# Kernel optimization log

Measured on AMD Instinct MI355X. Metric: run time of the kernel, lower is better.

Reference implementation:

```python
import jax, jax.numpy as jnp
import numpy as np

N = 524288      # total nodes across batched subgraphs
E = 4194304     # total edges (avg degree ~8)
B = 4096        # number of subgraphs (links)
H = 32          # hidden_dim
L = 3           # num_layers
K = 30          # sort-pool k
MAXZ = 1000     # max DRNL label
EPS = 1e-5      # BatchNorm eps


def setup_inputs() -> dict:
    key = jax.random.key(0)
    ks = jax.random.split(key, 12)
    x_z = jax.random.randint(ks[0], (N,), 0, MAXZ + 1, dtype=jnp.int32)
    edge_index = jax.random.randint(ks[1], (2, E), 0, N, dtype=jnp.int32)
    batch = jnp.sort(jax.random.randint(ks[2], (N,), 0, B, dtype=jnp.int32))
    # parameters
    emb = jax.random.normal(ks[3], (MAXZ + 1, H), jnp.float32) * 0.1
    Wc = jax.random.normal(ks[4], (L, H, H), jnp.float32) * (1.0 / np.sqrt(H))
    bc = jnp.zeros((L, H), jnp.float32)
    gamma = jnp.ones((L, H), jnp.float32)
    beta = jnp.zeros((L, H), jnp.float32)
    rmean = jax.random.normal(ks[5], (L, H), jnp.float32) * 0.1
    rvar = 1.0 + 0.1 * jax.random.uniform(ks[6], (L, H), jnp.float32)
    W1 = jax.random.normal(ks[7], (K * H, H), jnp.float32) * (1.0 / np.sqrt(K * H))
    b1 = jnp.zeros((H,), jnp.float32)
    W2 = jax.random.normal(ks[8], (H, H // 2), jnp.float32) * (1.0 / np.sqrt(H))
    b2 = jnp.zeros((H // 2,), jnp.float32)
    W3 = jax.random.normal(ks[9], (H // 2, 1), jnp.float32) * (1.0 / np.sqrt(H // 2))
    b3 = jnp.zeros((1,), jnp.float32)
    return dict(x_z=x_z, edge_index=edge_index, batch=batch, emb=emb, Wc=Wc, bc=bc,
                gamma=gamma, beta=beta, rmean=rmean, rvar=rvar,
                W1=W1, b1=b1, W2=W2, b2=b2, W3=W3, b3=b3)


def reference(x_z, edge_index, batch, emb, Wc, bc, gamma, beta, rmean, rvar,
              W1, b1, W2, b2, W3, b3):
    src, dst = edge_index[0], edge_index[1]
    # GCN symmetric normalization with added self-loops: deg[i] = in_deg(i) + 1
    deg = jnp.zeros((N,), jnp.float32).at[dst].add(1.0) + 1.0
    dinv = jax.lax.rsqrt(deg)
    enorm = dinv[src] * dinv[dst]          # [E]
    self_norm = dinv * dinv                # [N] self-loop coefficient

    x = emb[x_z]                           # [N, H]
    for i in range(L):
        h = x @ Wc[i]                      # [N, H]
        agg = (jnp.zeros_like(h).at[dst].add(h[src] * enorm[:, None])
               + h * self_norm[:, None] + bc[i])
        # BatchNorm1d (eval: running stats) + ReLU; dropout is identity in eval
        xn = (agg - rmean[i]) * jax.lax.rsqrt(rvar[i] + EPS) * gamma[i] + beta[i]
        x = jax.nn.relu(xn)

    # SortAggregation: per-graph sort desc by last channel, keep top-K, zero-pad
    order = jnp.lexsort((-x[:, -1], batch))   # group by graph, desc by last feat
    xs = x[order]
    bs = batch[order]
    counts = jnp.zeros((B,), jnp.int32).at[batch].add(1)
    starts = jnp.concatenate([jnp.zeros((1,), jnp.int32), jnp.cumsum(counts)[:-1]])
    rank = jnp.arange(N, dtype=jnp.int32) - starts[bs]
    slot = jnp.where(rank < K, rank, K)       # overflow -> dummy slot K
    pooled = jnp.zeros((B, K + 1, H), x.dtype).at[bs, slot].set(xs)
    pooled = pooled[:, :K].reshape(B, K * H)  # [B, K*H]

    h1 = jax.nn.relu(pooled @ W1 + b1)
    h2 = jax.nn.relu(h1 @ W2 + b2)
    out = (h2 @ W3 + b3)[:, 0]                # [B]
    return out
```

## Files before the change

kernel.cpp:

```cpp
#include <hip/hip_runtime.h>
#include <hip/hip_bf16.h>
#include <stdint.h>

#define N_NODES 524288
#define N_EDGES 4194304
#define N_GRAPHS 4096
#define HDIM 32
#define NLAYERS 3
#define KPOOL 30
#define MAXC 1024

#define NBUCKET 1024
#define BSHIFT 9
#define NPB 512
#define NCOPY 8
#define HIST_SZ (NBUCKET * NCOPY)
#define CAP 6144

typedef unsigned long long ull;

__global__ void k_hist(const int* __restrict__ dst, int* __restrict__ ghist,
                       int* __restrict__ deg) {
    __shared__ int lh[NBUCKET];
    int t = threadIdx.x;
    for (int i = t; i < NBUCKET; i += 256) lh[i] = 0;
    __syncthreads();
    int base = blockIdx.x * 2048;
    for (int i = t; i < 2048; i += 256) {
        int d = dst[base + i];
        atomicAdd(&lh[d >> BSHIFT], 1);
        atomicAdd(&deg[d], 1);
    }
    __syncthreads();
    int c = blockIdx.x & 7;
    for (int i = t; i < NBUCKET; i += 256) {
        int v = lh[i];
        if (v) atomicAdd(&ghist[i * NCOPY + c], v);
    }
}

__global__ void k_dinv(const int* __restrict__ deg, float* __restrict__ dinv) {
    int n = blockIdx.x * 256 + threadIdx.x;
    if (n < N_NODES) {
        float d = (float)(deg[n] + 1);
        float sq = (float)sqrt((double)d);
        dinv[n] = (float)(1.0 / (double)sq);
    }
}

__global__ void k_scan8k(const int* __restrict__ ghist, int* __restrict__ gbase,
                         int* __restrict__ cur) {
    __shared__ int tmp[256];
    int t = threadIdx.x;
    int loc[32];
    int s = 0;
    for (int k = 0; k < 32; ++k) { loc[k] = ghist[t * 32 + k]; s += loc[k]; }
    tmp[t] = s;
    __syncthreads();
    for (int d = 1; d < 256; d <<= 1) {
        int a = (t >= d) ? tmp[t - d] : 0;
        __syncthreads();
        tmp[t] += a;
        __syncthreads();
    }
    int run = tmp[t] - s;
    for (int k = 0; k < 32; ++k) {
        gbase[t * 32 + k] = run;
        cur[t * 32 + k] = run;
        run += loc[k];
    }
}

__global__ void k_bin(const int* __restrict__ src, const int* __restrict__ dst,
                      int* __restrict__ cur, ull* __restrict__ stage) {
    int base = blockIdx.x * 2048;
    int c = blockIdx.x & 7;
    int t = threadIdx.x;
    for (int i = t; i < 2048; i += 256) {
        int e = base + i;
        int d = dst[e];
        int b = d >> BSHIFT;
        int pos = atomicAdd(&cur[b * NCOPY + c], 1);
        ull rec = ((ull)(unsigned)src[e] << 32)
                | (unsigned)(((d & (NPB - 1)) << 22) | e);
        stage[pos] = rec;
    }
}

__global__ void k_build(const ull* __restrict__ stage, const int* __restrict__ gbase,
                        const float* __restrict__ dinv,
                        int* __restrict__ offs, ull* __restrict__ csr2,
                        int* __restrict__ perm) {
    __shared__ ull grp[CAP];
    __shared__ int cnt[NPB];
    __shared__ int sstart[NPB];
    __shared__ int cur[NPB];
    __shared__ int tmp[256];
    int b = blockIdx.x, t = threadIdx.x;
    int s0 = gbase[b * NCOPY];
    int s1 = (b == NBUCKET - 1) ? N_EDGES : gbase[(b + 1) * NCOPY];
    int win = s1 - s0;
    for (int j = t; j < NPB; j += 256) cnt[j] = 0;
    __syncthreads();
    const unsigned* lo32 = (const unsigned*)stage;
    for (int i = t; i < win; i += 256) {
        unsigned k = lo32[2 * (s0 + i)];
        atomicAdd(&cnt[(k >> 22) & (NPB - 1)], 1);
    }
    __syncthreads();
    int j0 = 2 * t, j1 = 2 * t + 1;
    int a0 = cnt[j0], a1 = cnt[j1];
    int s = a0 + a1;
    tmp[t] = s;
    __syncthreads();
    for (int d = 1; d < 256; d <<= 1) {
        int a = (t >= d) ? tmp[t - d] : 0;
        __syncthreads();
        tmp[t] += a;
        __syncthreads();
    }
    int run = tmp[t] - s;
    sstart[j0] = run;      sstart[j1] = run + a0;
    cur[j0] = run;         cur[j1] = run + a0;
    offs[b * NPB + j0] = s0 + run;
    offs[b * NPB + j1] = s0 + run + a0;
    if (b == NBUCKET - 1 && t == 255) offs[N_NODES] = N_EDGES;
    __syncthreads();

    if (win <= CAP) {
        for (int i = t; i < win; i += 256) {
            ull v = stage[s0 + i];
            unsigned k = (unsigned)v;
            int pos = atomicAdd(&cur[(k >> 22) & (NPB - 1)], 1);
            grp[pos] = v;
        }
        __syncthreads();
        for (int jj = 0; jj < 2; ++jj) {
            int j = 2 * t + jj;
            int beg = sstart[j], end = beg + cnt[j];
            for (int i = beg + 1; i < end; ++i) {
                ull v = grp[i];
                unsigned kv = (unsigned)v;
                int q = i - 1;
                while (q >= beg && (unsigned)grp[q] > kv) { grp[q + 1] = grp[q]; --q; }
                grp[q + 1] = v;
            }
        }
        __syncthreads();
        int i = t;
        for (; i + 768 < win; i += 1024) {
            ull v0 = grp[i], v1 = grp[i + 256], v2 = grp[i + 512], v3 = grp[i + 768];
            float d0 = dinv[(int)(v0 >> 32)];
            float d1 = dinv[(int)(v1 >> 32)];
            float d2 = dinv[(int)(v2 >> 32)];
            float d3 = dinv[(int)(v3 >> 32)];
            csr2[s0 + i]       = (v0 & 0xffffffff00000000ull) | (unsigned)__float_as_uint(d0);
            csr2[s0 + i + 256] = (v1 & 0xffffffff00000000ull) | (unsigned)__float_as_uint(d1);
            csr2[s0 + i + 512] = (v2 & 0xffffffff00000000ull) | (unsigned)__float_as_uint(d2);
            csr2[s0 + i + 768] = (v3 & 0xffffffff00000000ull) | (unsigned)__float_as_uint(d3);
        }
        for (; i < win; i += 256) {
            ull v = grp[i];
            float dv = dinv[(int)(v >> 32)];
            csr2[s0 + i] = (v & 0xffffffff00000000ull) | (unsigned)__float_as_uint(dv);
        }
    } else {
        for (int i = t; i < win; i += 256) {
            ull v = stage[s0 + i];
            unsigned k = (unsigned)v;
            int pos = s0 + atomicAdd(&cur[(k >> 22) & (NPB - 1)], 1);
            csr2[pos] = v;
        }
        __syncthreads();
        for (int jj = 0; jj < 2; ++jj) {
            int j = 2 * t + jj;
            int beg = s0 + sstart[j], end = beg + cnt[j];
            for (int i = beg + 1; i < end; ++i) {
                ull v = csr2[i];
                unsigned kv = (unsigned)v;
                int q = i - 1;
                while (q >= beg && (unsigned)csr2[q] > kv) { csr2[q + 1] = csr2[q]; --q; }
                csr2[q + 1] = v;
            }
        }
        __syncthreads();
        for (int i = t; i < win; i += 256) {
            ull v = csr2[s0 + i];
            float dv = dinv[(int)(v >> 32)];
            csr2[s0 + i] = (v & 0xffffffff00000000ull) | (unsigned)__float_as_uint(dv);
        }
    }
    __syncthreads();
    for (int jj = 0; jj < 2; ++jj) {
        int j = 2 * t + jj;
        int dj = cnt[j];
        int r = 0;
        for (int k = 0; k < NPB; ++k) {
            int dk = cnt[k];
            r += (dk < dj) || (dk == dj && k < j);
        }
        perm[b * NPB + r] = b * NPB + j;
    }
}

__global__ void k_bnprep(const float* __restrict__ rvar, float* __restrict__ rs) {
    int i = threadIdx.x;
    if (i < NLAYERS * HDIM) {
        float rv = __fadd_rn(rvar[i], 1e-5f);
        float sq = (float)sqrt((double)rv);
        rs[i] = (float)(1.0 / (double)sq);
    }
}

__global__ void k_embed_mm(const int* __restrict__ xz, const float* __restrict__ emb,
                           const float* __restrict__ Wc, float* __restrict__ h) {
    __shared__ float Wl[HDIM * HDIM];
    __shared__ float xt[256];
    int t = threadIdx.x;
    int base = blockIdx.x * 256;
    for (int i = t; i < HDIM * HDIM; i += 256) Wl[i] = Wc[i];
    {
        int gid = base + t;
        int n = gid >> 5, c = gid & 31;
        xt[t] = emb[xz[n] * HDIM + c];
    }
    __syncthreads();
    int nl = t >> 5, c = t & 31;
    float acc = 0.0f;
#pragma unroll
    for (int k = 0; k < HDIM; ++k) acc = __fmaf_rn(xt[nl * HDIM + k], Wl[k * HDIM + c], acc);
    h[base + t] = acc;
}

__device__ __forceinline__ float agg_phase(const float* __restrict__ h,
                                           const float* __restrict__ dinv,
                                           const int* __restrict__ offs,
                                           const ull* __restrict__ csr2,
                                           const float* __restrict__ bc,
                                           const float* __restrict__ rmean,
                                           const float* __restrict__ rs,
                                           const float* __restrict__ gamma,
                                           const float* __restrict__ beta,
                                           int n, int c) {
    float di = dinv[n];
    float hself = h[n * HDIM + c];
    float accE = 0.0f;
    int beg = offs[n], end = offs[n + 1];
    int i = beg;
    for (; i + 8 <= end; i += 8) {
        ull r0 = csr2[i];
        ull r1 = csr2[i + 1];
        ull r2 = csr2[i + 2];
        ull r3 = csr2[i + 3];
        ull r4 = csr2[i + 4];
        ull r5 = csr2[i + 5];
        ull r6 = csr2[i + 6];
        ull r7 = csr2[i + 7];
        float h0 = h[(int)(r0 >> 32) * HDIM + c];
        float h1 = h[(int)(r1 >> 32) * HDIM + c];
        float h2 = h[(int)(r2 >> 32) * HDIM + c];
        float h3 = h[(int)(r3 >> 32) * HDIM + c];
        float h4 = h[(int)(r4 >> 32) * HDIM + c];
        float h5 = h[(int)(r5 >> 32) * HDIM + c];
        float h6 = h[(int)(r6 >> 32) * HDIM + c];
        float h7 = h[(int)(r7 >> 32) * HDIM + c];
        accE = __fadd_rn(accE, __fmul_rn(h0, __fmul_rn(__uint_as_float((unsigned)r0), di)));
        accE = __fadd_rn(accE, __fmul_rn(h1, __fmul_rn(__uint_as_float((unsigned)r1), di)));
        accE = __fadd_rn(accE, __fmul_rn(h2, __fmul_rn(__uint_as_float((unsigned)r2), di)));
        accE = __fadd_rn(accE, __fmul_rn(h3, __fmul_rn(__uint_as_float((unsigned)r3), di)));
        accE = __fadd_rn(accE, __fmul_rn(h4, __fmul_rn(__uint_as_float((unsigned)r4), di)));
        accE = __fadd_rn(accE, __fmul_rn(h5, __fmul_rn(__uint_as_float((unsigned)r5), di)));
        accE = __fadd_rn(accE, __fmul_rn(h6, __fmul_rn(__uint_as_float((unsigned)r6), di)));
        accE = __fadd_rn(accE, __fmul_rn(h7, __fmul_rn(__uint_as_float((unsigned)r7), di)));
    }
    for (; i + 4 <= end; i += 4) {
        ull r0 = csr2[i];
        ull r1 = csr2[i + 1];
        ull r2 = csr2[i + 2];
        ull r3 = csr2[i + 3];
        float h0 = h[(int)(r0 >> 32) * HDIM + c];
        float h1 = h[(int)(r1 >> 32) * HDIM + c];
        float h2 = h[(int)(r2 >> 32) * HDIM + c];
        float h3 = h[(int)(r3 >> 32) * HDIM + c];
        accE = __fadd_rn(accE, __fmul_rn(h0, __fmul_rn(__uint_as_float((unsigned)r0), di)));
        accE = __fadd_rn(accE, __fmul_rn(h1, __fmul_rn(__uint_as_float((unsigned)r1), di)));
        accE = __fadd_rn(accE, __fmul_rn(h2, __fmul_rn(__uint_as_float((unsigned)r2), di)));
        accE = __fadd_rn(accE, __fmul_rn(h3, __fmul_rn(__uint_as_float((unsigned)r3), di)));
    }
    for (; i < end; ++i) {
        ull r = csr2[i];
        float hv = h[(int)(r >> 32) * HDIM + c];
        float dv = __uint_as_float((unsigned)r);
        accE = __fadd_rn(accE, __fmul_rn(hv, __fmul_rn(dv, di)));
    }
    float sn = __fmul_rn(di, di);
    float t1 = __fmul_rn(hself, sn);
    float a2 = __fadd_rn(accE, t1);
    float a3 = __fadd_rn(a2, bc[c]);
    float tt = __fsub_rn(a3, rmean[c]);
    float u  = __fmul_rn(tt, rs[c]);
    float v  = __fmul_rn(u, gamma[c]);
    float xn = __fadd_rn(v, beta[c]);
    return (xn > 0.0f) ? xn : 0.0f;
}

__global__ void k_agg_mm(const float* __restrict__ h, const float* __restrict__ dinv,
                         const int* __restrict__ offs, const ull* __restrict__ csr2,
                         const int* __restrict__ perm,
                         const float* __restrict__ bc, const float* __restrict__ rmean,
                         const float* __restrict__ rs, const float* __restrict__ gamma,
                         const float* __restrict__ beta,
                         const float* __restrict__ Wnext, float* __restrict__ hout) {
    __shared__ float Wl[HDIM * HDIM];
    __shared__ float xt[256];
    __shared__ int nodes[8];
    int t = threadIdx.x;
    for (int i = t; i < HDIM * HDIM; i += 256) Wl[i] = Wnext[i];
    if (t < 8) nodes[t] = perm[blockIdx.x * 8 + t];
    __syncthreads();
    int slot = t >> 5, c = t & 31;
    int n = nodes[slot];
    xt[t] = agg_phase(h, dinv, offs, csr2, bc, rmean, rs, gamma, beta, n, c);
    __syncthreads();
    float acc = 0.0f;
#pragma unroll
    for (int k = 0; k < HDIM; ++k) acc = __fmaf_rn(xt[slot * HDIM + k], Wl[k * HDIM + c], acc);
    hout[n * HDIM + c] = acc;
}

__global__ void k_agg_last(const float* __restrict__ h, const float* __restrict__ dinv,
                           const int* __restrict__ offs, const ull* __restrict__ csr2,
                           const int* __restrict__ perm,
                           const float* __restrict__ bc, const float* __restrict__ rmean,
                           const float* __restrict__ rs, const float* __restrict__ gamma,
                           const float* __restrict__ beta, float* __restrict__ xout,
                           float* __restrict__ lastc) {
    __shared__ int nodes[8];
    int t = threadIdx.x;
    if (t < 8) nodes[t] = perm[blockIdx.x * 8 + t];
    __syncthreads();
    int slot = t >> 5, c = t & 31;
    int n = nodes[slot];
    float v = agg_phase(h, dinv, offs, csr2, bc, rmean, rs, gamma, beta, n, c);
    xout[n * HDIM + c] = v;
    if (c == 31) lastc[n] = v;
}

__global__ void k_starts(const int* __restrict__ batch, int* __restrict__ start) {
    int n = blockIdx.x * 256 + threadIdx.x;
    if (n >= N_NODES) return;
    int bn = batch[n];
    int bp = (n == 0) ? -1 : batch[n - 1];
    for (int g = bp + 1; g <= bn; ++g) start[g] = n;
    if (n == N_NODES - 1) {
        for (int g = bn + 1; g <= N_GRAPHS; ++g) start[g] = N_NODES;
    }
}

__global__ void k_pool_mlp(const float* __restrict__ x, const float* __restrict__ lastc,
                           const int* __restrict__ start,
                           const float* __restrict__ W1, const float* __restrict__ b1,
                           const float* __restrict__ W2, const float* __restrict__ b2,
                           const float* __restrict__ W3, const float* __restrict__ b3,
                           float* __restrict__ out) {
    int g = blockIdx.x;
    int t = threadIdx.x;
    int s = start[g], e = start[g + 1];
    int cnt = e - s;

    __shared__ ull keys[MAXC];
    __shared__ int sel[KPOOL];
    __shared__ float pl[KPOOL * HDIM];
    __shared__ double part[64];
    __shared__ double h1[HDIM];
    __shared__ double h2[HDIM / 2];

    bool inlds = (cnt <= MAXC);
    if (inlds) {
        for (int i = t; i < cnt; i += 64) {
            int n = s + i;
            keys[i] = ((ull)__float_as_uint(lastc[n]) << 32) | (unsigned int)(~n);
        }
    }
    __syncthreads();

    ull prev = ~0ull;
    for (int k = 0; k < KPOOL; ++k) {
        if (k < cnt) {
            ull best = 0ull;
            if (inlds) {
                for (int i = t; i < cnt; i += 64) {
                    ull key = keys[i];
                    if (key < prev && key > best) best = key;
                }
            } else {
                for (int n = s + t; n < e; n += 64) {
                    ull key = ((ull)__float_as_uint(lastc[n]) << 32) | (unsigned int)(~n);
                    if (key < prev && key > best) best = key;
                }
            }
            for (int off = 32; off; off >>= 1) {
                ull o = __shfl_down(best, off);
                if (o > best) best = o;
            }
            best = __shfl(best, 0);
            prev = best;
            if (t == 0) sel[k] = (int)(~((unsigned int)(best & 0xffffffffull)));
        } else {
            if (t == 0) sel[k] = -1;
        }
    }
    __syncthreads();

    for (int idx = t; idx < KPOOL * HDIM; idx += 64) {
        int k = idx >> 5, c = idx & 31;
        int n = sel[k];
        pl[idx] = (n >= 0) ? x[n * HDIM + c] : 0.0f;
    }
    __syncthreads();

    {
        int j = t & 31;
        int half = t >> 5;
        double acc = 0.0;
        int r0 = half * (KPOOL * HDIM / 2);
        for (int r = r0; r < r0 + KPOOL * HDIM / 2; ++r)
            acc += (double)pl[r] * (double)W1[r * HDIM + j];
        part[t] = acc;
    }
    __syncthreads();
    if (t < HDIM) {
        double v = part[t] + part[t + 32] + (double)b1[t];
        h1[t] = (v > 0.0) ? v : 0.0;
    }
    __syncthreads();

    if (t < HDIM / 2) {
        double a2 = (double)b2[t];
        for (int i = 0; i < HDIM; ++i) a2 += h1[i] * (double)W2[i * (HDIM / 2) + t];
        h2[t] = (a2 > 0.0) ? a2 : 0.0;
    }
    __syncthreads();

    if (t == 0) {
        double o = (double)b3[0];
        for (int i = 0; i < HDIM / 2; ++i) o += h2[i] * (double)W3[i];
        out[g] = (float)o;
    }
}

extern "C" void kernel_launch(void* const* d_in, const int* in_sizes, int n_in,
                              void* d_out, int out_size, void* d_ws, size_t ws_size,
                              hipStream_t stream) {
    const int*   xz    = (const int*)d_in[0];
    const int*   src   = (const int*)d_in[1];
    const int*   dst   = (const int*)d_in[1] + N_EDGES;
    const int*   batch = (const int*)d_in[2];
    const float* emb   = (const float*)d_in[3];
    const float* Wc    = (const float*)d_in[4];
    const float* bc    = (const float*)d_in[5];
    const float* gamma = (const float*)d_in[6];
    const float* beta  = (const float*)d_in[7];
    const float* rmean = (const float*)d_in[8];
    const float* rvar  = (const float*)d_in[9];
    const float* W1    = (const float*)d_in[10];
    const float* b1    = (const float*)d_in[11];
    const float* W2    = (const float*)d_in[12];
    const float* b2    = (const float*)d_in[13];
    const float* W3    = (const float*)d_in[14];
    const float* b3    = (const float*)d_in[15];
    float* out = (float*)d_out;

    char* p = (char*)d_ws;
    auto carve = [&](size_t bytes) {
        void* q = (void*)p;
        p += (bytes + 255) & ~size_t(255);
        return q;
    };
    int*   ghist = (int*)carve(HIST_SZ * 4);
    int*   gbase = (int*)carve(HIST_SZ * 4);
    int*   cur   = (int*)carve(HIST_SZ * 4);
    int*   deg   = (int*)carve(N_NODES * 4);
    ull*   stage = (ull*)carve((size_t)N_EDGES * 8);
    ull*   csr2  = (ull*)carve((size_t)N_EDGES * 8);
    float* dinv  = (float*)carve(N_NODES * 4);
    int*   offs  = (int*)carve((N_NODES + 1) * 4);
    int*   permB = (int*)carve(N_NODES * 4);
    int*   start = (int*)carve((N_GRAPHS + 1) * 4);
    float* rs    = (float*)carve(NLAYERS * HDIM * 4);
    float* lastc = (float*)carve(N_NODES * 4);
    float* bufA  = (float*)carve((size_t)N_NODES * HDIM * 4);
    float* bufB  = (float*)carve((size_t)N_NODES * HDIM * 4);

    hipMemsetAsync(ghist, 0, HIST_SZ * 4, stream);
    hipMemsetAsync(deg, 0, N_NODES * 4, stream);

    k_hist<<<N_EDGES / 2048, 256, 0, stream>>>(dst, ghist, deg);
    k_scan8k<<<1, 256, 0, stream>>>(ghist, gbase, cur);
    k_dinv<<<N_NODES / 256, 256, 0, stream>>>(deg, dinv);
    k_bin<<<N_EDGES / 2048, 256, 0, stream>>>(src, dst, cur, stage);
    k_build<<<NBUCKET, 256, 0, stream>>>(stage, gbase, dinv, offs, csr2, permB);
    k_bnprep<<<1, 128, 0, stream>>>(rvar, rs);
    k_starts<<<N_NODES / 256, 256, 0, stream>>>(batch, start);

    const int NG = (N_NODES * HDIM) / 256;
    k_embed_mm<<<NG, 256, 0, stream>>>(xz, emb, Wc + 0 * HDIM * HDIM, bufA);
    k_agg_mm<<<N_NODES / 8, 256, 0, stream>>>(bufA, dinv, offs, csr2, permB,
        bc + 0 * HDIM, rmean + 0 * HDIM, rs + 0 * HDIM, gamma + 0 * HDIM, beta + 0 * HDIM,
        Wc + 1 * HDIM * HDIM, bufB);
    k_agg_mm<<<N_NODES / 8, 256, 0, stream>>>(bufB, dinv, offs, csr2, permB,
        bc + 1 * HDIM, rmean + 1 * HDIM, rs + 1 * HDIM, gamma + 1 * HDIM, beta + 1 * HDIM,
        Wc + 2 * HDIM * HDIM, bufA);
    k_agg_last<<<N_NODES / 8, 256, 0, stream>>>(bufA, dinv, offs, csr2, permB,
        bc + 2 * HDIM, rmean + 2 * HDIM, rs + 2 * HDIM, gamma + 2 * HDIM, beta + 2 * HDIM,
        bufB, lastc);

    k_pool_mlp<<<N_GRAPHS, 64, 0, stream>>>(bufB, lastc, start, W1, b1, W2, b2, W3, b3, out);
}
```

Baseline: 1.277 ms.

## Derive degrees from bucket counts in k_build and pack dinv in separate pass

```diff
diff --git a/kernel.cpp b/kernel.cpp
--- a/kernel.cpp
+++ b/kernel.cpp
@@ -19,8 +19,7 @@
 
 typedef unsigned long long ull;
 
-__global__ void k_hist(const int* __restrict__ dst, int* __restrict__ ghist,
-                       int* __restrict__ deg) {
+__global__ void k_hist(const int* __restrict__ dst, int* __restrict__ ghist) {
     __shared__ int lh[NBUCKET];
     int t = threadIdx.x;
     for (int i = t; i < NBUCKET; i += 256) lh[i] = 0;
@@ -29,22 +28,12 @@
     for (int i = t; i < 2048; i += 256) {
         int d = dst[base + i];
         atomicAdd(&lh[d >> BSHIFT], 1);
-        atomicAdd(&deg[d], 1);
     }
     __syncthreads();
     int c = blockIdx.x & 7;
     for (int i = t; i < NBUCKET; i += 256) {
         int v = lh[i];
         if (v) atomicAdd(&ghist[i * NCOPY + c], v);
-    }
-}
-
-__global__ void k_dinv(const int* __restrict__ deg, float* __restrict__ dinv) {
-    int n = blockIdx.x * 256 + threadIdx.x;
-    if (n < N_NODES) {
-        float d = (float)(deg[n] + 1);
-        float sq = (float)sqrt((double)d);
-        dinv[n] = (float)(1.0 / (double)sq);
     }
 }
 
@@ -88,7 +77,7 @@
 }
 
 __global__ void k_build(const ull* __restrict__ stage, const int* __restrict__ gbase,
-                        const float* __restrict__ dinv,
+                        float* __restrict__ dinv,
                         int* __restrict__ offs, ull* __restrict__ csr2,
                         int* __restrict__ perm) {
     __shared__ ull grp[CAP];
@@ -110,6 +99,14 @@
     __syncthreads();
     int j0 = 2 * t, j1 = 2 * t + 1;
     int a0 = cnt[j0], a1 = cnt[j1];
+    {
+        float d0 = (float)(a0 + 1);
+        float q0 = (float)sqrt((double)d0);
+        dinv[b * NPB + j0] = (float)(1.0 / (double)q0);
+        float d1 = (float)(a1 + 1);
+        float q1 = (float)sqrt((double)d1);
+        dinv[b * NPB + j1] = (float)(1.0 / (double)q1);
+    }
     int s = a0 + a1;
     tmp[t] = s;
     __syncthreads();
@@ -147,23 +144,7 @@
             }
         }
         __syncthreads();
-        int i = t;
-        for (; i + 768 < win; i += 1024) {
-            ull v0 = grp[i], v1 = grp[i + 256], v2 = grp[i + 512], v3 = grp[i + 768];
-            float d0 = dinv[(int)(v0 >> 32)];
-            float d1 = dinv[(int)(v1 >> 32)];
-            float d2 = dinv[(int)(v2 >> 32)];
-            float d3 = dinv[(int)(v3 >> 32)];
-            csr2[s0 + i]       = (v0 & 0xffffffff00000000ull) | (unsigned)__float_as_uint(d0);
-            csr2[s0 + i + 256] = (v1 & 0xffffffff00000000ull) | (unsigned)__float_as_uint(d1);
-            csr2[s0 + i + 512] = (v2 & 0xffffffff00000000ull) | (unsigned)__float_as_uint(d2);
-            csr2[s0 + i + 768] = (v3 & 0xffffffff00000000ull) | (unsigned)__float_as_uint(d3);
-        }
-        for (; i < win; i += 256) {
-            ull v = grp[i];
-            float dv = dinv[(int)(v >> 32)];
-            csr2[s0 + i] = (v & 0xffffffff00000000ull) | (unsigned)__float_as_uint(dv);
-        }
+        for (int i = t; i < win; i += 256) csr2[s0 + i] = grp[i];
     } else {
         for (int i = t; i < win; i += 256) {
             ull v = stage[s0 + i];
@@ -183,12 +164,6 @@
                 csr2[q + 1] = v;
             }
         }
-        __syncthreads();
-        for (int i = t; i < win; i += 256) {
-            ull v = csr2[s0 + i];
-            float dv = dinv[(int)(v >> 32)];
-            csr2[s0 + i] = (v & 0xffffffff00000000ull) | (unsigned)__float_as_uint(dv);
-        }
     }
     __syncthreads();
     for (int jj = 0; jj < 2; ++jj) {
@@ -200,6 +175,15 @@
             r += (dk < dj) || (dk == dj && k < j);
         }
         perm[b * NPB + r] = b * NPB + j;
+    }
+}
+
+__global__ void k_pack(const float* __restrict__ dinv, ull* __restrict__ csr2) {
+    int i = blockIdx.x * 256 + threadIdx.x;
+    if (i < N_EDGES) {
+        ull r = csr2[i];
+        int s = (int)(r >> 32);
+        csr2[i] = (r & 0xffffffff00000000ull) | (unsigned)__float_as_uint(dinv[s]);
     }
 }
 
@@ -480,7 +464,6 @@
     int*   ghist = (int*)carve(HIST_SZ * 4);
     int*   gbase = (int*)carve(HIST_SZ * 4);
     int*   cur   = (int*)carve(HIST_SZ * 4);
-    int*   deg   = (int*)carve(N_NODES * 4);
     ull*   stage = (ull*)carve((size_t)N_EDGES * 8);
     ull*   csr2  = (ull*)carve((size_t)N_EDGES * 8);
     float* dinv  = (float*)carve(N_NODES * 4);
@@ -493,13 +476,12 @@
     float* bufB  = (float*)carve((size_t)N_NODES * HDIM * 4);
 
     hipMemsetAsync(ghist, 0, HIST_SZ * 4, stream);
-    hipMemsetAsync(deg, 0, N_NODES * 4, stream);
-
-    k_hist<<<N_EDGES / 2048, 256, 0, stream>>>(dst, ghist, deg);
+
+    k_hist<<<N_EDGES / 2048, 256, 0, stream>>>(dst, ghist);
     k_scan8k<<<1, 256, 0, stream>>>(ghist, gbase, cur);
-    k_dinv<<<N_NODES / 256, 256, 0, stream>>>(deg, dinv);
     k_bin<<<N_EDGES / 2048, 256, 0, stream>>>(src, dst, cur, stage);
     k_build<<<NBUCKET, 256, 0, stream>>>(stage, gbase, dinv, offs, csr2, permB);
+    k_pack<<<N_EDGES / 256, 256, 0, stream>>>(dinv, csr2);
     k_bnprep<<<1, 128, 0, stream>>>(rvar, rs);
     k_starts<<<N_NODES / 256, 256, 0, stream>>>(batch, start);
 
```

After: 1.145 ms. 10.3% less time.

## Derive node degrees from bucketed counts instead of global atomics

Applied to the files above, without the earlier changes.

```diff
diff --git a/kernel.cpp b/kernel.cpp
--- a/kernel.cpp
+++ b/kernel.cpp
@@ -19,8 +19,8 @@
 
 typedef unsigned long long ull;
 
-__global__ void k_hist(const int* __restrict__ dst, int* __restrict__ ghist,
-                       int* __restrict__ deg) {
+
+__global__ void k_hist(const int* __restrict__ dst, int* __restrict__ ghist) {
     __shared__ int lh[NBUCKET];
     int t = threadIdx.x;
     for (int i = t; i < NBUCKET; i += 256) lh[i] = 0;
@@ -29,22 +29,12 @@
     for (int i = t; i < 2048; i += 256) {
         int d = dst[base + i];
         atomicAdd(&lh[d >> BSHIFT], 1);
-        atomicAdd(&deg[d], 1);
     }
     __syncthreads();
     int c = blockIdx.x & 7;
     for (int i = t; i < NBUCKET; i += 256) {
         int v = lh[i];
-        if (v) atomicAdd(&ghist[i * NCOPY + c], v);
-    }
-}
-
-__global__ void k_dinv(const int* __restrict__ deg, float* __restrict__ dinv) {
-    int n = blockIdx.x * 256 + threadIdx.x;
-    if (n < N_NODES) {
-        float d = (float)(deg[n] + 1);
-        float sq = (float)sqrt((double)d);
-        dinv[n] = (float)(1.0 / (double)sq);
+        if (v) atomicAdd(&ghist[c * NBUCKET + i], v);
     }
 }
 
@@ -54,7 +44,12 @@
     int t = threadIdx.x;
     int loc[32];
     int s = 0;
-    for (int k = 0; k < 32; ++k) { loc[k] = ghist[t * 32 + k]; s += loc[k]; }
+    for (int k = 0; k < 32; ++k) {
+        int r = t * 32 + k;
+        int idx = (r & 7) * NBUCKET + (r >> 3);
+        loc[k] = ghist[idx];
+        s += loc[k];
+    }
     tmp[t] = s;
     __syncthreads();
     for (int d = 1; d < 256; d <<= 1) {
@@ -65,8 +60,10 @@
     }
     int run = tmp[t] - s;
     for (int k = 0; k < 32; ++k) {
-        gbase[t * 32 + k] = run;
-        cur[t * 32 + k] = run;
+        int r = t * 32 + k;
+        int idx = (r & 7) * NBUCKET + (r >> 3);
+        gbase[idx] = run;
+        cur[idx] = run;
         run += loc[k];
     }
 }
@@ -80,25 +77,21 @@
         int e = base + i;
         int d = dst[e];
         int b = d >> BSHIFT;
-        int pos = atomicAdd(&cur[b * NCOPY + c], 1);
+        int pos = atomicAdd(&cur[c * NBUCKET + b], 1);
         ull rec = ((ull)(unsigned)src[e] << 32)
                 | (unsigned)(((d & (NPB - 1)) << 22) | e);
         stage[pos] = rec;
     }
 }
 
-__global__ void k_build(const ull* __restrict__ stage, const int* __restrict__ gbase,
-                        const float* __restrict__ dinv,
-                        int* __restrict__ offs, ull* __restrict__ csr2,
-                        int* __restrict__ perm) {
-    __shared__ ull grp[CAP];
+__global__ void k_cnt(const ull* __restrict__ stage, const int* __restrict__ gbase,
+                      float* __restrict__ dinv, int* __restrict__ offs,
+                      int* __restrict__ perm) {
     __shared__ int cnt[NPB];
-    __shared__ int sstart[NPB];
-    __shared__ int cur[NPB];
     __shared__ int tmp[256];
     int b = blockIdx.x, t = threadIdx.x;
-    int s0 = gbase[b * NCOPY];
-    int s1 = (b == NBUCKET - 1) ? N_EDGES : gbase[(b + 1) * NCOPY];
+    int s0 = gbase[b];
+    int s1 = (b == NBUCKET - 1) ? N_EDGES : gbase[b + 1];
     int win = s1 - s0;
     for (int j = t; j < NPB; j += 256) cnt[j] = 0;
     __syncthreads();
@@ -110,6 +103,14 @@
     __syncthreads();
     int j0 = 2 * t, j1 = 2 * t + 1;
     int a0 = cnt[j0], a1 = cnt[j1];
+    {
+        float d0 = (float)(a0 + 1);
+        float q0 = (float)sqrt((double)d0);
+        dinv[b * NPB + j0] = (float)(1.0 / (double)q0);
+        float d1 = (float)(a1 + 1);
+        float q1 = (float)sqrt((double)d1);
+        dinv[b * NPB + j1] = (float)(1.0 / (double)q1);
+    }
     int s = a0 + a1;
     tmp[t] = s;
     __syncthreads();
@@ -120,24 +121,50 @@
         __syncthreads();
     }
     int run = tmp[t] - s;
-    sstart[j0] = run;      sstart[j1] = run + a0;
-    cur[j0] = run;         cur[j1] = run + a0;
     offs[b * NPB + j0] = s0 + run;
     offs[b * NPB + j1] = s0 + run + a0;
     if (b == NBUCKET - 1 && t == 255) offs[N_NODES] = N_EDGES;
+    __syncthreads();
+    for (int jj = 0; jj < 2; ++jj) {
+        int j = 2 * t + jj;
+        int dj = cnt[j];
+        int r = 0;
+        for (int k = 0; k < NPB; ++k) {
+            int dk = cnt[k];
+            r += (dk < dj) || (dk == dj && k < j);
+        }
+        perm[b * NPB + r] = b * NPB + j;
+    }
+}
+
+__global__ void k_build2(const ull* __restrict__ stage, const int* __restrict__ gbase,
+                         const int* __restrict__ offs, const float* __restrict__ dinv,
+                         ull* __restrict__ csr2) {
+    __shared__ ull grp[CAP];
+    __shared__ int sstart[NPB];
+    __shared__ int scur[NPB];
+    int b = blockIdx.x, t = threadIdx.x;
+    int s0 = gbase[b];
+    int s1 = (b == NBUCKET - 1) ? N_EDGES : gbase[b + 1];
+    int win = s1 - s0;
+    for (int j = t; j < NPB; j += 256) {
+        int v = offs[b * NPB + j] - s0;
+        sstart[j] = v;
+        scur[j] = v;
+    }
     __syncthreads();
 
     if (win <= CAP) {
         for (int i = t; i < win; i += 256) {
             ull v = stage[s0 + i];
             unsigned k = (unsigned)v;
-            int pos = atomicAdd(&cur[(k >> 22) & (NPB - 1)], 1);
+            int pos = atomicAdd(&scur[(k >> 22) & (NPB - 1)], 1);
             grp[pos] = v;
         }
         __syncthreads();
         for (int jj = 0; jj < 2; ++jj) {
             int j = 2 * t + jj;
-            int beg = sstart[j], end = beg + cnt[j];
+            int beg = sstart[j], end = scur[j];
             for (int i = beg + 1; i < end; ++i) {
                 ull v = grp[i];
                 unsigned kv = (unsigned)v;
@@ -168,13 +195,13 @@
         for (int i = t; i < win; i += 256) {
             ull v = stage[s0 + i];
             unsigned k = (unsigned)v;
-            int pos = s0 + atomicAdd(&cur[(k >> 22) & (NPB - 1)], 1);
+            int pos = s0 + atomicAdd(&scur[(k >> 22) & (NPB - 1)], 1);
             csr2[pos] = v;
         }
         __syncthreads();
         for (int jj = 0; jj < 2; ++jj) {
             int j = 2 * t + jj;
-            int beg = s0 + sstart[j], end = beg + cnt[j];
+            int beg = s0 + sstart[j], end = s0 + scur[j];
             for (int i = beg + 1; i < end; ++i) {
                 ull v = csr2[i];
                 unsigned kv = (unsigned)v;
@@ -189,17 +216,6 @@
             float dv = dinv[(int)(v >> 32)];
             csr2[s0 + i] = (v & 0xffffffff00000000ull) | (unsigned)__float_as_uint(dv);
         }
-    }
-    __syncthreads();
-    for (int jj = 0; jj < 2; ++jj) {
-        int j = 2 * t + jj;
-        int dj = cnt[j];
-        int r = 0;
-        for (int k = 0; k < NPB; ++k) {
-            int dk = cnt[k];
-            r += (dk < dj) || (dk == dj && k < j);
-        }
-        perm[b * NPB + r] = b * NPB + j;
     }
 }
 
@@ -480,7 +496,6 @@
     int*   ghist = (int*)carve(HIST_SZ * 4);
     int*   gbase = (int*)carve(HIST_SZ * 4);
     int*   cur   = (int*)carve(HIST_SZ * 4);
-    int*   deg   = (int*)carve(N_NODES * 4);
     ull*   stage = (ull*)carve((size_t)N_EDGES * 8);
     ull*   csr2  = (ull*)carve((size_t)N_EDGES * 8);
     float* dinv  = (float*)carve(N_NODES * 4);
@@ -493,13 +508,12 @@
     float* bufB  = (float*)carve((size_t)N_NODES * HDIM * 4);
 
     hipMemsetAsync(ghist, 0, HIST_SZ * 4, stream);
-    hipMemsetAsync(deg, 0, N_NODES * 4, stream);
-
-    k_hist<<<N_EDGES / 2048, 256, 0, stream>>>(dst, ghist, deg);
+
+    k_hist<<<N_EDGES / 2048, 256, 0, stream>>>(dst, ghist);
     k_scan8k<<<1, 256, 0, stream>>>(ghist, gbase, cur);
-    k_dinv<<<N_NODES / 256, 256, 0, stream>>>(deg, dinv);
     k_bin<<<N_EDGES / 2048, 256, 0, stream>>>(src, dst, cur, stage);
-    k_build<<<NBUCKET, 256, 0, stream>>>(stage, gbase, dinv, offs, csr2, permB);
+    k_cnt<<<NBUCKET, 256, 0, stream>>>(stage, gbase, dinv, offs, permB);
+    k_build2<<<NBUCKET, 256, 0, stream>>>(stage, gbase, offs, dinv, csr2);
     k_bnprep<<<1, 128, 0, stream>>>(rvar, rs);
     k_starts<<<N_NODES / 256, 256, 0, stream>>>(batch, start);
 
```

Measured after the change: 1.121 ms. 12.2% less time.
